# Performance work log

Hardware: AMD Instinct MI355X
Metric: run time of the kernel (lower is better)

The kernel has to match this reference:

```python
import jax, jax.numpy as jnp
import numpy as np

# Irrep structure (fixed by init_kwargs):
#   irreps_in      = 128x0e + 128x1o          -> x: [N, 128 + 128*3] = [N, 512]
#   irreps_nonlin  = 32x0e + 16x1o            (16 scalars + 16 gates + 16 gated vectors)
#   hidden_irreps  = 16x0e + 16x1o            (Gate output)
#   irreps_out     = 10x0e + 1x1o             -> out: [N, 13]
MUL_IN = 128
N_SCAL = 16   # gated-block scalars
N_GATE = 16   # gate scalars
N_VEC = 16    # gated 1o multiplicity
NUM_ELEM = 10


def setup_inputs() -> dict:
    key = jax.random.key(0)
    ks = jax.random.split(key, 8)
    N = 100000
    x = jax.random.normal(ks[0], (N, MUL_IN * 4), dtype=jnp.float32)  # 128 scalars + 128 vectors
    # o3.Linear weights: N(0,1) init, one (mul_in, mul_out) block per matching irrep pair
    W1_s = jax.random.normal(ks[1], (MUL_IN, N_SCAL + N_GATE), dtype=jnp.float32)  # 128x0e -> 32x0e
    W1_v = jax.random.normal(ks[2], (MUL_IN, N_VEC), dtype=jnp.float32)            # 128x1o -> 16x1o
    b1_s = jax.random.normal(ks[3], (N_SCAL + N_GATE,), dtype=jnp.float32) * 0.1   # bias on 0e only
    W2_s = jax.random.normal(ks[4], (N_SCAL, NUM_ELEM), dtype=jnp.float32)         # 16x0e -> 10x0e
    W2_v = jax.random.normal(ks[5], (N_VEC, 1), dtype=jnp.float32)                 # 16x1o -> 1x1o
    b2_s = jax.random.normal(ks[6], (NUM_ELEM,), dtype=jnp.float32) * 0.1
    return {"x": x, "W1_s": W1_s, "W1_v": W1_v, "b1_s": b1_s,
            "W2_s": W2_s, "W2_v": W2_v, "b2_s": b2_s}


def reference(x, W1_s, W1_v, b1_s, W2_s, W2_v, b2_s):
    N = x.shape[0]
    inv1 = 1.0 / np.sqrt(MUL_IN)   # o3.Linear path normalization (single path per output)
    inv2s = 1.0 / np.sqrt(N_SCAL)
    inv2v = 1.0 / np.sqrt(N_VEC)

    x_s = x[:, :MUL_IN]                               # [N, 128] scalars (0e)
    x_v = x[:, MUL_IN:].reshape(N, MUL_IN, 3)         # [N, 128, 3] vectors (1o)

    # linear_1: irreps_in -> irreps_nonlin (bias on scalar outputs only)
    h_s = x_s @ W1_s * inv1 + b1_s                    # [N, 32]
    h_v = jnp.einsum('nic,io->noc', x_v, W1_v) * inv1 # [N, 16, 3]

    # Gate: silu on scalars; silu(gates) elementwise-scales gated vectors
    scalars = jax.nn.silu(h_s[:, :N_SCAL])            # [N, 16]
    gates = jax.nn.silu(h_s[:, N_SCAL:])              # [N, 16]
    gated_v = gates[:, :, None] * h_v                 # [N, 16, 3]

    # linear_2: hidden_irreps -> irreps_out (10x0e + 1x1o)
    out_s = scalars @ W2_s * inv2s + b2_s             # [N, 10]
    out_v = jnp.einsum('nic,io->noc', gated_v, W2_v) * inv2v  # [N, 1, 3]
    return jnp.concatenate([out_s, out_v.reshape(N, 3)], axis=-1)  # [N, 13]
```

## Files before the change

### kernel.cpp

```cpp
#include <hip/hip_runtime.h>
#include <math.h>


typedef short  bf16x8 __attribute__((ext_vector_type(8)));
typedef float  f32x4  __attribute__((ext_vector_type(4)));

static __device__ __forceinline__ short f2bf(float f) {
    union { float f; unsigned u; } v; v.f = f;
    return (short)((v.u + 0x8000u) >> 16);
}

#define BLOCK 256

__global__ __launch_bounds__(BLOCK, 2) void nlrb_kernel(
    const float* __restrict__ x,
    const float* __restrict__ W1s,
    const float* __restrict__ W1v,
    const float* __restrict__ b1s,
    const float* __restrict__ W2s,
    const float* __restrict__ W2v,
    const float* __restrict__ b2s,
    float* __restrict__ out,
    int N)
{
    __shared__ float sred[4][16][68];

    const int tid  = threadIdx.x;
    const int wave = tid >> 6;
    const int lane = tid & 63;
    const int mq   = lane >> 4;
    const int o    = lane & 15;
    const float inv1 = 0.08838834764831843f;

    bf16x8 bS0[4], bS1[4], bV[4];
    #pragma unroll
    for (int kb = 0; kb < 4; ++kb) {
        #pragma unroll
        for (int j = 0; j < 8; ++j) {
            const int k = kb * 32 + mq * 8 + j;
            bS0[kb][j] = f2bf(W1s[k * 32 + o]);
            bS1[kb][j] = f2bf(W1s[k * 32 + 16 + o]);
            bV [kb][j] = f2bf(W1v[k * 16 + o]);
        }
    }
    const int e = o;
    float wcr[16];
    #pragma unroll
    for (int j = 0; j < 16; ++j)
        wcr[j] = (e < 10) ? W2s[j * 10 + e] : W2v[j];
    const float b2e = (e < 10) ? b2s[e] : 0.0f;
    const float b1a = b1s[o];
    const float b1b = b1s[16 + o];

    const int NT = N >> 4;
    const int wstride = gridDim.x << 2;

    for (int wt = (blockIdx.x << 2) + wave; wt < NT; wt += wstride) {
        const int base = wt << 4;
        const float* xp = x + (size_t)(base + o) * 512;

        float4 LS[4][2], LV[4][6];
        #pragma unroll
        for (int kb = 0; kb < 4; ++kb) {
            LS[kb][0] = *(const float4*)(xp + kb * 32 + mq * 8);
            LS[kb][1] = *(const float4*)(xp + kb * 32 + mq * 8 + 4);
        }
        #pragma unroll
        for (int kb = 0; kb < 4; ++kb) {
            #pragma unroll
            for (int q = 0; q < 6; ++q)
                LV[kb][q] = *(const float4*)(xp + 128 + kb * 96 + mq * 24 + q * 4);
        }

        f32x4 accS0 = {0.f,0.f,0.f,0.f}, accS1 = {0.f,0.f,0.f,0.f};
        f32x4 accV0 = {0.f,0.f,0.f,0.f}, accV1 = {0.f,0.f,0.f,0.f};
        f32x4 accV2 = {0.f,0.f,0.f,0.f};

        #pragma unroll
        for (int kb = 0; kb < 4; ++kb) {
            float u[8];
            u[0]=LS[kb][0].x; u[1]=LS[kb][0].y; u[2]=LS[kb][0].z; u[3]=LS[kb][0].w;
            u[4]=LS[kb][1].x; u[5]=LS[kb][1].y; u[6]=LS[kb][1].z; u[7]=LS[kb][1].w;
            bf16x8 a;
            #pragma unroll
            for (int j = 0; j < 8; ++j) a[j] = f2bf(u[j]);
            accS0 = __builtin_amdgcn_mfma_f32_16x16x32_bf16(a, bS0[kb], accS0, 0, 0, 0);
            accS1 = __builtin_amdgcn_mfma_f32_16x16x32_bf16(a, bS1[kb], accS1, 0, 0, 0);
        }
        #pragma unroll
        for (int kb = 0; kb < 4; ++kb) {
            float t[24];
            #pragma unroll
            for (int q = 0; q < 6; ++q) {
                t[4*q+0] = LV[kb][q].x; t[4*q+1] = LV[kb][q].y;
                t[4*q+2] = LV[kb][q].z; t[4*q+3] = LV[kb][q].w;
            }
            bf16x8 a0, a1, a2;
            #pragma unroll
            for (int j = 0; j < 8; ++j) {
                a0[j] = f2bf(t[3*j+0]);
                a1[j] = f2bf(t[3*j+1]);
                a2[j] = f2bf(t[3*j+2]);
            }
            accV0 = __builtin_amdgcn_mfma_f32_16x16x32_bf16(a0, bV[kb], accV0, 0, 0, 0);
            accV1 = __builtin_amdgcn_mfma_f32_16x16x32_bf16(a1, bV[kb], accV1, 0, 0, 0);
            accV2 = __builtin_amdgcn_mfma_f32_16x16x32_bf16(a2, bV[kb], accV2, 0, 0, 0);
        }

        #pragma unroll
        for (int v = 0; v < 4; ++v) {
            const float hs = fmaf(accS0[v], inv1, b1a);
            const float hg = fmaf(accS1[v], inv1, b1b);
            const float s  = hs / (1.f + __expf(-hs));
            const float g  = hg / (1.f + __expf(-hg));
            const float gm = g * inv1;
            const int  r   = mq * 4 + v;
            sred[wave][r][o]      = s;
            sred[wave][r][16 + o] = gm * accV0[v];
            sred[wave][r][32 + o] = gm * accV1[v];
            sred[wave][r][48 + o] = gm * accV2[v];
        }
        asm volatile("s_waitcnt lgkmcnt(0)" ::: "memory");

        #pragma unroll
        for (int w = 0; w < 4; ++w) {
            const int r = (w << 2) + mq;
            if (e < 13) {
                const int slot = (e < 10) ? 0 : (e - 9);
                const float* p = &sred[wave][r][slot * 16];
                float sum = 0.f;
                #pragma unroll
                for (int j = 0; j < 16; ++j)
                    sum = fmaf(p[j], wcr[j], sum);
                out[(size_t)(base + r) * 13 + e] = fmaf(sum, 0.25f, b2e);
            }
        }
        asm volatile("s_waitcnt lgkmcnt(0)" ::: "memory");
    }
}

extern "C" void kernel_launch(void* const* d_in, const int* in_sizes, int n_in,
                              void* d_out, int out_size, void* d_ws, size_t ws_size,
                              hipStream_t stream) {
    const float* x   = (const float*)d_in[0];
    const float* W1s = (const float*)d_in[1];
    const float* W1v = (const float*)d_in[2];
    const float* b1s = (const float*)d_in[3];
    const float* W2s = (const float*)d_in[4];
    const float* W2v = (const float*)d_in[5];
    const float* b2s = (const float*)d_in[6];
    float* outp = (float*)d_out;
    const int N = in_sizes[0] / 512;
    nlrb_kernel<<<dim3(512), dim3(BLOCK), 0, stream>>>(
        x, W1s, W1v, b1s, W2s, W2v, b2s, outp, N);
}
```

Measured before the change: 41.80 us.

## Software-pipeline next tile's x loads and use packed bf16 conversion

Restructures the grid-stride loop so each wave issues global loads for its next tile right after converting the current tile's registers, overlapping memory latency with MFMA work. It also replaces scalar rounding-based bf16 conversion with the v_cvt_pk_bf16_f32 packed instruction plus byte permutes to de-interleave vector components. The second-layer reduction reads shared memory as float4. The prefetch adds register pressure under launch_bounds(256,2), and the packed conversion may round differently from the manual helper.

```diff
diff --git a/kernel.cpp b/kernel.cpp
--- a/kernel.cpp
+++ b/kernel.cpp
@@ -3,11 +3,17 @@
 
 
 typedef short  bf16x8 __attribute__((ext_vector_type(8)));
+typedef int    i32x4  __attribute__((ext_vector_type(4)));
 typedef float  f32x4  __attribute__((ext_vector_type(4)));
 
 static __device__ __forceinline__ short f2bf(float f) {
     union { float f; unsigned u; } v; v.f = f;
     return (short)((v.u + 0x8000u) >> 16);
+}
+static __device__ __forceinline__ unsigned cvtpk(float lo, float hi) {
+    unsigned r;
+    asm("v_cvt_pk_bf16_f32 %0, %1, %2" : "=v"(r) : "v"(lo), "v"(hi));
+    return r;
 }
 
 #define BLOCK 256
@@ -43,100 +49,131 @@
             bV [kb][j] = f2bf(W1v[k * 16 + o]);
         }
     }
-    const int e = o;
     float wcr[16];
     #pragma unroll
     for (int j = 0; j < 16; ++j)
-        wcr[j] = (e < 10) ? W2s[j * 10 + e] : W2v[j];
-    const float b2e = (e < 10) ? b2s[e] : 0.0f;
+        wcr[j] = (o < 10) ? W2s[j * 10 + o] : W2v[j];
+    const float b2e = (o < 10) ? b2s[o] : 0.0f;
     const float b1a = b1s[o];
     const float b1b = b1s[16 + o];
 
     const int NT = N >> 4;
     const int wstride = gridDim.x << 2;
+    const int wt0 = (blockIdx.x << 2) + wave;
 
-    for (int wt = (blockIdx.x << 2) + wave; wt < NT; wt += wstride) {
+    float4 LS[4][2], LV[4][6];
+
+#define ISSUE_S(kb, xp)                                                      \
+    do {                                                                     \
+        LS[kb][0] = *(const float4*)((xp) + (kb) * 32 + mq * 8);             \
+        LS[kb][1] = *(const float4*)((xp) + (kb) * 32 + mq * 8 + 4);         \
+    } while (0)
+#define ISSUE_V(kb, xp)                                                      \
+    do {                                                                     \
+        _Pragma("unroll")                                                    \
+        for (int q = 0; q < 6; ++q)                                          \
+            LV[kb][q] = *(const float4*)((xp) + 128 + (kb) * 96 + mq * 24 + q * 4); \
+    } while (0)
+
+#define TILE_BODY(PF)                                                        \
+    do {                                                                     \
+        f32x4 accS0 = {0.f,0.f,0.f,0.f}, accS1 = {0.f,0.f,0.f,0.f};          \
+        f32x4 accV0 = {0.f,0.f,0.f,0.f}, accV1 = {0.f,0.f,0.f,0.f};          \
+        f32x4 accV2 = {0.f,0.f,0.f,0.f};                                     \
+                 \
+        _Pragma("unroll")                                                    \
+        for (int kb = 0; kb < 4; ++kb) {                                     \
+            i32x4 wv;                                                        \
+            wv[0] = (int)cvtpk(LS[kb][0].x, LS[kb][0].y);                    \
+            wv[1] = (int)cvtpk(LS[kb][0].z, LS[kb][0].w);                    \
+            wv[2] = (int)cvtpk(LS[kb][1].x, LS[kb][1].y);                    \
+            wv[3] = (int)cvtpk(LS[kb][1].z, LS[kb][1].w);                    \
+            if (PF) ISSUE_S(kb, xq);                                         \
+            const bf16x8 a = __builtin_bit_cast(bf16x8, wv);                 \
+            accS0 = __builtin_amdgcn_mfma_f32_16x16x32_bf16(a, bS0[kb], accS0, 0, 0, 0); \
+            accS1 = __builtin_amdgcn_mfma_f32_16x16x32_bf16(a, bS1[kb], accS1, 0, 0, 0); \
+        }                                                                    \
+           \
+        _Pragma("unroll")                                                    \
+        for (int kb = 0; kb < 4; ++kb) {                                     \
+            unsigned p[12];                                                  \
+            _Pragma("unroll")                                                \
+            for (int q = 0; q < 6; ++q) {                                    \
+                p[2*q]   = cvtpk(LV[kb][q].x, LV[kb][q].y);                  \
+                p[2*q+1] = cvtpk(LV[kb][q].z, LV[kb][q].w);                  \
+            }                                                                \
+            if (PF) ISSUE_V(kb, xq);                                         \
+            i32x4 w0, w1, w2;                                                \
+            _Pragma("unroll")                                                \
+            for (int w = 0; w < 4; ++w) {                                    \
+                w0[w] = (int)__builtin_amdgcn_perm(p[3*w+1], p[3*w],   0x07060100u); \
+                w1[w] = (int)__builtin_amdgcn_perm(p[3*w+2], p[3*w],   0x05040302u); \
+                w2[w] = (int)__builtin_amdgcn_perm(p[3*w+2], p[3*w+1], 0x07060100u); \
+            }                                                                \
+            const bf16x8 a0 = __builtin_bit_cast(bf16x8, w0);                \
+            const bf16x8 a1 = __builtin_bit_cast(bf16x8, w1);                \
+            const bf16x8 a2 = __builtin_bit_cast(bf16x8, w2);                \
+            accV0 = __builtin_amdgcn_mfma_f32_16x16x32_bf16(a0, bV[kb], accV0, 0, 0, 0); \
+            accV1 = __builtin_amdgcn_mfma_f32_16x16x32_bf16(a1, bV[kb], accV1, 0, 0, 0); \
+            accV2 = __builtin_amdgcn_mfma_f32_16x16x32_bf16(a2, bV[kb], accV2, 0, 0, 0); \
+        }                                                                    \
+                             \
+        _Pragma("unroll")                                                    \
+        for (int v = 0; v < 4; ++v) {                                        \
+            const float hs = fmaf(accS0[v], inv1, b1a);                      \
+            const float hg = fmaf(accS1[v], inv1, b1b);                      \
+            const float s  = hs / (1.f + __expf(-hs));                       \
+            const float g  = hg / (1.f + __expf(-hg));                       \
+            const float gm = g * inv1;                                       \
+            const int  r   = mq * 4 + v;                                     \
+            sred[wave][r][o]      = s;                                       \
+            sred[wave][r][16 + o] = gm * accV0[v];                           \
+            sred[wave][r][32 + o] = gm * accV1[v];                           \
+            sred[wave][r][48 + o] = gm * accV2[v];                           \
+        }                                                                    \
+        asm volatile("s_waitcnt lgkmcnt(0)" ::: "memory");                   \
+              \
+        _Pragma("unroll")                                                    \
+        for (int w = 0; w < 4; ++w) {                                        \
+            const int r = (w << 2) + mq;                                     \
+            if (o < 13) {                                                    \
+                const int slot = (o < 10) ? 0 : (o - 9);                     \
+                const float* sp = &sred[wave][r][slot * 16];                 \
+                float sum = 0.f;                                             \
+                _Pragma("unroll")                                            \
+                for (int q = 0; q < 4; ++q) {                                \
+                    const float4 pv = *(const float4*)(sp + q * 4);          \
+                    sum = fmaf(pv.x, wcr[q * 4 + 0], sum);                   \
+                    sum = fmaf(pv.y, wcr[q * 4 + 1], sum);                   \
+                    sum = fmaf(pv.z, wcr[q * 4 + 2], sum);                   \
+                    sum = fmaf(pv.w, wcr[q * 4 + 3], sum);                   \
+                }                                                            \
+                out[(size_t)(base + r) * 13 + o] = fmaf(sum, 0.25f, b2e);    \
+            }                                                                \
+        }                                                                    \
+        asm volatile("s_waitcnt lgkmcnt(0)" ::: "memory");                   \
+    } while (0)
+
+    if (wt0 < NT) {
+        const float* xp = x + (size_t)((wt0 << 4) + o) * 512;
+        #pragma unroll
+        for (int kb = 0; kb < 4; ++kb) { ISSUE_S(kb, xp); ISSUE_V(kb, xp); }
+    }
+
+    int wt = wt0;
+    for (; wt + wstride < NT; wt += wstride) {
         const int base = wt << 4;
-        const float* xp = x + (size_t)(base + o) * 512;
-
-        float4 LS[4][2], LV[4][6];
-        #pragma unroll
-        for (int kb = 0; kb < 4; ++kb) {
-            LS[kb][0] = *(const float4*)(xp + kb * 32 + mq * 8);
-            LS[kb][1] = *(const float4*)(xp + kb * 32 + mq * 8 + 4);
-        }
-        #pragma unroll
-        for (int kb = 0; kb < 4; ++kb) {
-            #pragma unroll
-            for (int q = 0; q < 6; ++q)
-                LV[kb][q] = *(const float4*)(xp + 128 + kb * 96 + mq * 24 + q * 4);
-        }
-
-        f32x4 accS0 = {0.f,0.f,0.f,0.f}, accS1 = {0.f,0.f,0.f,0.f};
-        f32x4 accV0 = {0.f,0.f,0.f,0.f}, accV1 = {0.f,0.f,0.f,0.f};
-        f32x4 accV2 = {0.f,0.f,0.f,0.f};
-
-        #pragma unroll
-        for (int kb = 0; kb < 4; ++kb) {
-            float u[8];
-            u[0]=LS[kb][0].x; u[1]=LS[kb][0].y; u[2]=LS[kb][0].z; u[3]=LS[kb][0].w;
-            u[4]=LS[kb][1].x; u[5]=LS[kb][1].y; u[6]=LS[kb][1].z; u[7]=LS[kb][1].w;
-            bf16x8 a;
-            #pragma unroll
-            for (int j = 0; j < 8; ++j) a[j] = f2bf(u[j]);
-            accS0 = __builtin_amdgcn_mfma_f32_16x16x32_bf16(a, bS0[kb], accS0, 0, 0, 0);
-            accS1 = __builtin_amdgcn_mfma_f32_16x16x32_bf16(a, bS1[kb], accS1, 0, 0, 0);
-        }
-        #pragma unroll
-        for (int kb = 0; kb < 4; ++kb) {
-            float t[24];
-            #pragma unroll
-            for (int q = 0; q < 6; ++q) {
-                t[4*q+0] = LV[kb][q].x; t[4*q+1] = LV[kb][q].y;
-                t[4*q+2] = LV[kb][q].z; t[4*q+3] = LV[kb][q].w;
-            }
-            bf16x8 a0, a1, a2;
-            #pragma unroll
-            for (int j = 0; j < 8; ++j) {
-                a0[j] = f2bf(t[3*j+0]);
-                a1[j] = f2bf(t[3*j+1]);
-                a2[j] = f2bf(t[3*j+2]);
-            }
-            accV0 = __builtin_amdgcn_mfma_f32_16x16x32_bf16(a0, bV[kb], accV0, 0, 0, 0);
-            accV1 = __builtin_amdgcn_mfma_f32_16x16x32_bf16(a1, bV[kb], accV1, 0, 0, 0);
-            accV2 = __builtin_amdgcn_mfma_f32_16x16x32_bf16(a2, bV[kb], accV2, 0, 0, 0);
-        }
-
-        #pragma unroll
-        for (int v = 0; v < 4; ++v) {
-            const float hs = fmaf(accS0[v], inv1, b1a);
-            const float hg = fmaf(accS1[v], inv1, b1b);
-            const float s  = hs / (1.f + __expf(-hs));
-            const float g  = hg / (1.f + __expf(-hg));
-            const float gm = g * inv1;
-            const int  r   = mq * 4 + v;
-            sred[wave][r][o]      = s;
-            sred[wave][r][16 + o] = gm * accV0[v];
-            sred[wave][r][32 + o] = gm * accV1[v];
-            sred[wave][r][48 + o] = gm * accV2[v];
-        }
-        asm volatile("s_waitcnt lgkmcnt(0)" ::: "memory");
-
-        #pragma unroll
-        for (int w = 0; w < 4; ++w) {
-            const int r = (w << 2) + mq;
-            if (e < 13) {
-                const int slot = (e < 10) ? 0 : (e - 9);
-                const float* p = &sred[wave][r][slot * 16];
-                float sum = 0.f;
-                #pragma unroll
-                for (int j = 0; j < 16; ++j)
-                    sum = fmaf(p[j], wcr[j], sum);
-                out[(size_t)(base + r) * 13 + e] = fmaf(sum, 0.25f, b2e);
-            }
-        }
-        asm volatile("s_waitcnt lgkmcnt(0)" ::: "memory");
+        const float* xq = x + (size_t)(((wt + wstride) << 4) + o) * 512;
+        TILE_BODY(1);
     }
+    if (wt < NT) {
+        const int base = wt << 4;
+        const float* xq = nullptr; (void)xq;
+        TILE_BODY(0);
+    }
+#undef ISSUE_S
+#undef ISSUE_V
+#undef TILE_BODY
 }
 
 extern "C" void kernel_launch(void* const* d_in, const int* in_sizes, int n_in,
```

Measured after the change: 40.33 us, median of 2. 3.5% less time.
